# Optimization experiments

Measured on AMD Instinct MI355X. Metric: run time of the kernel, lower is better.

## Reference

```python
import jax, jax.numpy as jnp
import numpy as np

N = 100001          # 1000 DAGs * (99 tasks + 1 summary) + 1 global node
E = 3200000
IN_DIM = 8
H = 64
N_DAGS = 1000
TEMPERATURE = 1.0


def setup_inputs() -> dict:
    key = jax.random.key(0)
    ks = jax.random.split(key, 12)
    x = jax.random.normal(ks[0], (N, IN_DIM), dtype=jnp.float32)
    flags = jax.random.bernoulli(ks[1], 0.5, (N,)).astype(jnp.float32)
    x = x.at[:, -1].set(flags)  # last feature column is the schedule flag
    edge_index = jax.random.randint(ks[2], (2, E), 0, N, dtype=jnp.int32)
    dag_summary_index = jnp.arange(N_DAGS, dtype=jnp.int32) * 100 + 99

    def w(k, shape, fan_in):
        return jax.random.normal(k, shape, dtype=jnp.float32) / np.float32(np.sqrt(fan_in))

    return {
        'x': x,
        'edge_index': edge_index,
        'dag_summary_index': dag_summary_index,
        'W1': w(ks[3], (IN_DIM, H), IN_DIM), 'b1': jnp.zeros((H,), jnp.float32),
        'W2': w(ks[4], (H, H), H),           'b2': jnp.zeros((H,), jnp.float32),
        'M1': w(ks[5], (3 * H, H), 3 * H),   'mb1': jnp.zeros((H,), jnp.float32),
        'M2': w(ks[6], (H, H), H),           'mb2': jnp.zeros((H,), jnp.float32),
        'M3': w(ks[7], (H, 1), H),           'mb3': jnp.zeros((1,), jnp.float32),
    }


def _gcn_conv(x, src, dst, W, b):
    # PyG GCNConv: add self-loops, symmetric normalization, linear, scatter-add, bias
    n = x.shape[0]
    loop = jnp.arange(n, dtype=src.dtype)
    s = jnp.concatenate([src, loop])
    d = jnp.concatenate([dst, loop])
    deg = jax.ops.segment_sum(jnp.ones_like(s, dtype=x.dtype), d, num_segments=n)
    dinv = jnp.where(deg > 0, jax.lax.rsqrt(deg), 0.0)
    norm = dinv[s] * dinv[d]                      # [E+N]
    h = x @ W                                     # [N, H]
    msg = h[s] * norm[:, None]                    # gather + scale (memory-bound)
    return jax.ops.segment_sum(msg, d, num_segments=n) + b


def reference(x, edge_index, dag_summary_index, W1, b1, W2, b2, M1, mb1, M2, mb2, M3, mb3):
    src, dst = edge_index[0], edge_index[1]
    h = jax.nn.relu(_gcn_conv(x, src, dst, W1, b1))
    h = jax.nn.relu(_gcn_conv(h, src, dst, W2, b2))   # [N, H]

    n = x.shape[0]
    idx = jnp.arange(n - 1)
    # dag_idx for node i == number of summary indices <= i (matches loop increment)
    dag_of = jnp.searchsorted(dag_summary_index, idx, side='right')
    dag_of = jnp.clip(dag_of, 0, dag_summary_index.shape[0] - 1)
    dag_emb = h[dag_summary_index[dag_of]]            # [N-1, H]
    global_emb = jnp.broadcast_to(h[-1], (n - 1, h.shape[1]))
    combined = jnp.concatenate([h[:-1], dag_emb, global_emb], axis=1)  # [N-1, 3H]

    z = jax.nn.relu(combined @ M1 + mb1)
    z = jax.nn.relu(z @ M2 + mb2)
    scores = (z @ M3 + mb3)[:, 0]                     # [N-1]

    flags = x[:-1, -1]
    is_summary = jnp.zeros((n,), bool).at[dag_summary_index].set(True)[:-1]
    mask = (flags == 1.0) & (~is_summary)
    probs = jax.nn.softmax(jnp.where(mask, scores / TEMPERATURE, -jnp.inf))
    selected = jnp.argmax(probs)                      # is_sampling=False path
    return probs, selected
```

## Files before the change

kernel.cpp:

```cpp
#include <hip/hip_runtime.h>
#include <math.h>

#define CHUNK 8192


__global__ void __launch_bounds__(256) k_bcount(const int* __restrict__ dst, int e,
                                                int* __restrict__ bcount) {
    __shared__ int c[256];
    int t = threadIdx.x;
    c[t] = 0;
    __syncthreads();
    for (int i = blockIdx.x * 256 + t; i < e; i += gridDim.x * 256)
        atomicAdd(&c[dst[i] >> 9], 1);
    __syncthreads();
    if (c[t]) atomicAdd(&bcount[t], c[t]);
}

__global__ void k_bscan(const int* __restrict__ bcount, int nb, int e,
                        int* __restrict__ bbase, int* __restrict__ bcur) {
    __shared__ int s[256];
    int t = threadIdx.x;
    int v = (t < nb) ? bcount[t] : 0;
    s[t] = v;
    __syncthreads();
    for (int d = 1; d < 256; d <<= 1) {
        int a = (t >= d) ? s[t - d] : 0;
        __syncthreads();
        s[t] += a;
        __syncthreads();
    }
    if (t < nb) { bbase[t] = s[t] - v; bcur[t] = s[t] - v; }
    if (t == 0) bbase[nb] = e;
}

__global__ void __launch_bounds__(256) k_bscatter(const int* __restrict__ src,
                                                  const int* __restrict__ dst, int e,
                                                  int* __restrict__ bcur,
                                                  unsigned* __restrict__ eu) {
    __shared__ unsigned short rank[CHUNK];
    __shared__ int cnt[256];
    __shared__ int base[256];
    int t = threadIdx.x;
    int c0 = blockIdx.x * CHUNK;
    cnt[t] = 0;
    __syncthreads();
#pragma unroll
    for (int k = 0; k < CHUNK / 256; k++) {
        int i = c0 + k * 256 + t;
        if (i < e) {
            int b = dst[i] >> 9;
            rank[k * 256 + t] = (unsigned short)atomicAdd(&cnt[b], 1);
        }
    }
    __syncthreads();
    int cb = cnt[t];
    base[t] = cb ? atomicAdd(&bcur[t], cb) : 0;
    __syncthreads();
#pragma unroll
    for (int k = 0; k < CHUNK / 256; k++) {
        int i = c0 + k * 256 + t;
        if (i < e) {
            int d = dst[i];
            int b = d >> 9;
            eu[base[b] + rank[k * 256 + t]] =
                ((unsigned)src[i] << 9) | (unsigned)(d & 511);
        }
    }
}

__global__ void __launch_bounds__(256) k_bdeg(const unsigned* __restrict__ eu,
                                              const int* __restrict__ bbase,
                                              int* __restrict__ deg, int* __restrict__ off,
                                              float* __restrict__ dinv, int n) {
    __shared__ int h[512];
    int t = threadIdx.x, b = blockIdx.x;
    h[t] = 0; h[t + 256] = 0;
    __syncthreads();
    int s0 = bbase[b], s1 = bbase[b + 1];
    for (int i = s0 + t; i < s1; i += 256)
        atomicAdd(&h[eu[i] & 511u], 1);
    __syncthreads();
    int o0 = h[t], o1 = h[t + 256];
    for (int d = 1; d < 512; d <<= 1) {
        int a0 = (t >= d) ? h[t - d] : 0;
        int a1 = (t + 256 >= d) ? h[t + 256 - d] : 0;
        __syncthreads();
        h[t] += a0; h[t + 256] += a1;
        __syncthreads();
    }
    int nbase = b << 9;
    int n0 = nbase + t, n1 = nbase + t + 256;
    if (n0 < n) { deg[n0] = o0; off[n0] = s0 + h[t] - o0; dinv[n0] = rsqrtf((float)(o0 + 1)); }
    if (n1 < n) { deg[n1] = o1; off[n1] = s0 + h[t + 256] - o1; dinv[n1] = rsqrtf((float)(o1 + 1)); }
}

__global__ void __launch_bounds__(256) k_bcsr(const unsigned* __restrict__ eu,
                                              const int* __restrict__ bbase,
                                              const int* __restrict__ off,
                                              int* __restrict__ csr, int n) {
    __shared__ int curL[512];
    __shared__ int offL[512];
    int t = threadIdx.x, b = blockIdx.x;
    int nbase = b << 9;
    curL[t] = 0; curL[t + 256] = 0;
    int n0 = nbase + t, n1 = nbase + t + 256;
    offL[t] = (n0 < n) ? off[n0] : 0;
    offL[t + 256] = (n1 < n) ? off[n1] : 0;
    __syncthreads();
    int s0 = bbase[b], s1 = bbase[b + 1];
    for (int i = s0 + t; i < s1; i += 256) {
        unsigned p = eu[i];
        int local = (int)(p & 511u);
        int r = atomicAdd(&curL[local], 1);
        csr[offL[local] + r] = (int)(p >> 9);
    }
}


__global__ void k_xs(const float* __restrict__ x, const float* __restrict__ dinv,
                     float* __restrict__ xs, int n) {
    int t = blockIdx.x * blockDim.x + threadIdx.x;
    if (t >= n * 8) return;
    xs[t] = x[t] * dinv[t >> 3];
}


__global__ void __launch_bounds__(256) k_conv8(const float* __restrict__ xs,
                                               const int* __restrict__ csr,
                                               const int* __restrict__ off,
                                               const int* __restrict__ deg,
                                               float* __restrict__ agg1, int n) {
    int g = (blockIdx.x * 256 + threadIdx.x) >> 3;
    int lane = threadIdx.x & 7;
    if (g >= n) return;
    int base = off[g], cnt = deg[g];
    float acc = xs[g * 8 + lane];
    int e = 0;
    for (; e + 4 <= cnt; e += 4) {
        int s0 = csr[base + e];
        int s1 = csr[base + e + 1];
        int s2 = csr[base + e + 2];
        int s3 = csr[base + e + 3];
        acc += xs[s0 * 8 + lane];
        acc += xs[s1 * 8 + lane];
        acc += xs[s2 * 8 + lane];
        acc += xs[s3 * 8 + lane];
    }
    for (; e < cnt; e++) acc += xs[csr[base + e] * 8 + lane];
    agg1[g * 8 + lane] = acc;
}


__global__ void k_h1(const float* __restrict__ agg1, const float* __restrict__ W1,
                     const float* __restrict__ b1, const float* __restrict__ dinv,
                     float* __restrict__ H1s, int n) {
    int t = blockIdx.x * blockDim.x + threadIdx.x;
    int i = t >> 6, j = t & 63;
    if (i >= n) return;
    const float* ar = agg1 + (size_t)i * 8;
    float acc = 0.f;
#pragma unroll
    for (int k = 0; k < 8; k++) acc += ar[k] * W1[k * 64 + j];
    float dv = dinv[i];
    float h = fmaxf(dv * acc + b1[j], 0.f);
    H1s[(size_t)i * 64 + j] = h * dv;
}


__global__ void __launch_bounds__(256) k_conv64(const float* __restrict__ G,
                                                const int* __restrict__ csr,
                                                const int* __restrict__ off,
                                                const int* __restrict__ deg,
                                                float* __restrict__ agg2, int n) {
    int d = (blockIdx.x * 256 + threadIdx.x) >> 6;
    int j = threadIdx.x & 63;
    if (d >= n) return;
    int du = __builtin_amdgcn_readfirstlane(d);
    int base = off[du], cnt = deg[du];
    const float* Gj = G + j;
    float acc = Gj[(size_t)du * 64];
    int e = 0;
    for (; e + 8 <= cnt; e += 8) {
        int s[8];
#pragma unroll
        for (int u = 0; u < 8; u++) s[u] = csr[base + e + u];
        float v[8];
#pragma unroll
        for (int u = 0; u < 8; u++) v[u] = Gj[(size_t)s[u] * 64];
#pragma unroll
        for (int u = 0; u < 8; u++) acc += v[u];
    }
    for (; e < cnt; e++) acc += Gj[(size_t)csr[base + e] * 64];
    agg2[(size_t)d * 64 + j] = acc;
}


__global__ void __launch_bounds__(256) k_gw2b(const float* __restrict__ In,
                                              const float* __restrict__ W2,
                                              const float* __restrict__ b2,
                                              const float* __restrict__ dinv,
                                              float* __restrict__ Out, int n) {
    __shared__ float hs[128 * 65];
    __shared__ float ws[64 * 64];
    int tid = threadIdx.x;
    int base = blockIdx.x * 128;
#pragma unroll
    for (int m = 0; m < 4; m++) {
        int i = (m * 256 + tid) * 4;
        *(float4*)&ws[i] = *(const float4*)&W2[i];
    }
#pragma unroll
    for (int m = 0; m < 8; m++) {
        int idx = (m * 256 + tid) * 4;
        int node = idx >> 6, k = idx & 63;
        float4 v = *(const float4*)&In[(size_t)(base + node) * 64 + k];
        hs[node * 65 + k]     = v.x;
        hs[node * 65 + k + 1] = v.y;
        hs[node * 65 + k + 2] = v.z;
        hs[node * 65 + k + 3] = v.w;
    }
    __syncthreads();
    int jg = tid & 7, ng = tid >> 3;
    int j0 = jg * 8, n0 = ng * 4;
    float acc[4][8];
#pragma unroll
    for (int i = 0; i < 4; i++)
#pragma unroll
        for (int j = 0; j < 8; j++) acc[i][j] = 0.f;
#pragma unroll 4
    for (int k = 0; k < 64; k++) {
        float av[4];
#pragma unroll
        for (int i = 0; i < 4; i++) av[i] = hs[(n0 + i) * 65 + k];
        float bv[8];
        *(float4*)&bv[0] = *(float4*)&ws[k * 64 + j0];
        *(float4*)&bv[4] = *(float4*)&ws[k * 64 + j0 + 4];
#pragma unroll
        for (int i = 0; i < 4; i++)
#pragma unroll
            for (int j = 0; j < 8; j++) acc[i][j] += av[i] * bv[j];
    }
    float b2v[8];
    *(float4*)&b2v[0] = *(const float4*)&b2[j0];
    *(float4*)&b2v[4] = *(const float4*)&b2[j0 + 4];
#pragma unroll
    for (int i = 0; i < 4; i++) {
        int node = base + n0 + i;
        if (node < n) {
            float dv = dinv[node];
            float4 o0, o1;
            o0.x = fmaxf(acc[i][0] * dv + b2v[0], 0.f);
            o0.y = fmaxf(acc[i][1] * dv + b2v[1], 0.f);
            o0.z = fmaxf(acc[i][2] * dv + b2v[2], 0.f);
            o0.w = fmaxf(acc[i][3] * dv + b2v[3], 0.f);
            o1.x = fmaxf(acc[i][4] * dv + b2v[4], 0.f);
            o1.y = fmaxf(acc[i][5] * dv + b2v[5], 0.f);
            o1.z = fmaxf(acc[i][6] * dv + b2v[6], 0.f);
            o1.w = fmaxf(acc[i][7] * dv + b2v[7], 0.f);
            *(float4*)&Out[(size_t)node * 64 + j0]     = o0;
            *(float4*)&Out[(size_t)node * 64 + j0 + 4] = o1;
        }
    }
}


__global__ void k_dgt(const float* __restrict__ Hfin, const int* __restrict__ dsi,
                      const float* __restrict__ M1, const float* __restrict__ b1,
                      float* __restrict__ dgt, int n, int nd) {
    int w = (blockIdx.x * blockDim.x + threadIdx.x) >> 6;
    int lane = threadIdx.x & 63;
    if (w >= nd) return;
    float hd = Hfin[(size_t)dsi[w] * 64 + lane];
    float hg = Hfin[(size_t)(n - 1) * 64 + lane];
    float z = b1[lane];
#pragma unroll
    for (int k = 0; k < 64; k++) z += __shfl(hd, k) * M1[(64 + k) * 64 + lane];
#pragma unroll
    for (int k = 0; k < 64; k++) z += __shfl(hg, k) * M1[(128 + k) * 64 + lane];
    dgt[w * 64 + lane] = z;
}


__global__ void __launch_bounds__(256) k_mlp(const float* __restrict__ Hfin,
                                             const float* __restrict__ dgt,
                                             const float* __restrict__ x,
                                             const float* __restrict__ M1,
                                             const float* __restrict__ M2,
                                             const float* __restrict__ mb2,
                                             const float* __restrict__ M3,
                                             const float* __restrict__ mb3,
                                             float* __restrict__ scores, int n, int nd) {
    __shared__ float hs[128 * 65];
    __shared__ float ws[64 * 64];
    int tid = threadIdx.x;
    int base = blockIdx.x * 128;
#pragma unroll
    for (int m = 0; m < 4; m++) {
        int i = (m * 256 + tid) * 4;
        *(float4*)&ws[i] = *(const float4*)&M1[i];
    }
#pragma unroll
    for (int m = 0; m < 8; m++) {
        int idx = (m * 256 + tid) * 4;
        int node = idx >> 6, k = idx & 63;
        float4 v = *(const float4*)&Hfin[(size_t)(base + node) * 64 + k];
        hs[node * 65 + k]     = v.x;
        hs[node * 65 + k + 1] = v.y;
        hs[node * 65 + k + 2] = v.z;
        hs[node * 65 + k + 3] = v.w;
    }
    __syncthreads();
    int jg = tid & 7, ng = tid >> 3;
    int j0 = jg * 8, n0 = ng * 4;
    float acc[4][8];
#pragma unroll
    for (int i = 0; i < 4; i++)
#pragma unroll
        for (int j = 0; j < 8; j++) acc[i][j] = 0.f;
#pragma unroll 4
    for (int k = 0; k < 64; k++) {
        float av[4];
#pragma unroll
        for (int i = 0; i < 4; i++) av[i] = hs[(n0 + i) * 65 + k];
        float bv[8];
        *(float4*)&bv[0] = *(float4*)&ws[k * 64 + j0];
        *(float4*)&bv[4] = *(float4*)&ws[k * 64 + j0 + 4];
#pragma unroll
        for (int i = 0; i < 4; i++)
#pragma unroll
            for (int j = 0; j < 8; j++) acc[i][j] += av[i] * bv[j];
    }
    __syncthreads();
#pragma unroll
    for (int i = 0; i < 4; i++) {
        int node = base + n0 + i;
        int dago = (node + 1) / 100;
        if (dago >= nd) dago = nd - 1;
        float dv[8];
        *(float4*)&dv[0] = *(const float4*)&dgt[dago * 64 + j0];
        *(float4*)&dv[4] = *(const float4*)&dgt[dago * 64 + j0 + 4];
#pragma unroll
        for (int j = 0; j < 8; j++)
            hs[(n0 + i) * 65 + j0 + j] = fmaxf(acc[i][j] + dv[j], 0.f);
    }
#pragma unroll
    for (int m = 0; m < 4; m++) {
        int i = (m * 256 + tid) * 4;
        *(float4*)&ws[i] = *(const float4*)&M2[i];
    }
    __syncthreads();
    float acc2[4][8];
#pragma unroll
    for (int i = 0; i < 4; i++)
#pragma unroll
        for (int j = 0; j < 8; j++) acc2[i][j] = 0.f;
#pragma unroll 4
    for (int k = 0; k < 64; k++) {
        float av[4];
#pragma unroll
        for (int i = 0; i < 4; i++) av[i] = hs[(n0 + i) * 65 + k];
        float bv[8];
        *(float4*)&bv[0] = *(float4*)&ws[k * 64 + j0];
        *(float4*)&bv[4] = *(float4*)&ws[k * 64 + j0 + 4];
#pragma unroll
        for (int i = 0; i < 4; i++)
#pragma unroll
            for (int j = 0; j < 8; j++) acc2[i][j] += av[i] * bv[j];
    }
    float b2v[8], m3v[8];
    *(float4*)&b2v[0] = *(const float4*)&mb2[j0];
    *(float4*)&b2v[4] = *(const float4*)&mb2[j0 + 4];
    *(float4*)&m3v[0] = *(const float4*)&M3[j0];
    *(float4*)&m3v[4] = *(const float4*)&M3[j0 + 4];
    float b3 = mb3[0];
#pragma unroll
    for (int i = 0; i < 4; i++) {
        float p = 0.f;
#pragma unroll
        for (int j = 0; j < 8; j++) {
            float z2 = fmaxf(acc2[i][j] + b2v[j], 0.f);
            p += z2 * m3v[j];
        }
        p += __shfl_xor(p, 1);
        p += __shfl_xor(p, 2);
        p += __shfl_xor(p, 4);
        if (jg == 0) {
            int node = base + n0 + i;
            if (node < n - 1) {
                float flag = x[(size_t)node * 8 + 7];
                bool summary = ((node % 100) == 99);
                scores[node] = (flag == 1.0f && !summary) ? (p + b3) : -INFINITY;
            }
        }
    }
}


__global__ void k_red_ms(const float* __restrict__ scores, int n,
                         float* __restrict__ pm, float* __restrict__ ps,
                         int* __restrict__ pidx) {
    __shared__ float sm[256];
    __shared__ float ss[256];
    __shared__ int si[256];
    float m = -INFINITY, s = 0.f;
    int bi = 0x7fffffff;
    for (int i = blockIdx.x * 256 + threadIdx.x; i < n; i += gridDim.x * 256) {
        float v = scores[i];
        if (v > m) {
            s = s * expf(m - v) + 1.f;
            m = v;
            bi = i;
        } else if (v != -INFINITY) {
            s += expf(v - m);
        }
    }
    sm[threadIdx.x] = m; ss[threadIdx.x] = s; si[threadIdx.x] = bi;
    __syncthreads();
    for (int o = 128; o; o >>= 1) {
        if (threadIdx.x < o) {
            float m2 = sm[threadIdx.x + o], s2 = ss[threadIdx.x + o];
            int i2 = si[threadIdx.x + o];
            float m1 = sm[threadIdx.x], s1 = ss[threadIdx.x];
            int i1 = si[threadIdx.x];
            float M = fmaxf(m1, m2);
            float S = ((m1 == -INFINITY) ? 0.f : s1 * expf(m1 - M)) +
                      ((m2 == -INFINITY) ? 0.f : s2 * expf(m2 - M));
            int I;
            if (m2 > m1 || (m2 == m1 && i2 < i1)) I = i2; else I = i1;
            sm[threadIdx.x] = M; ss[threadIdx.x] = S; si[threadIdx.x] = I;
        }
        __syncthreads();
    }
    if (threadIdx.x == 0) { pm[blockIdx.x] = sm[0]; ps[blockIdx.x] = ss[0]; pidx[blockIdx.x] = si[0]; }
}

__global__ void k_red_comb(const float* __restrict__ pm, const float* __restrict__ ps,
                           const int* __restrict__ pidx, int nb,
                           float* __restrict__ finals, int* __restrict__ seli) {
    __shared__ float sm[256];
    __shared__ float ss[256];
    __shared__ int si[256];
    int t = threadIdx.x;
    sm[t] = (t < nb) ? pm[t] : -INFINITY;
    ss[t] = (t < nb) ? ps[t] : 0.f;
    si[t] = (t < nb) ? pidx[t] : 0x7fffffff;
    __syncthreads();
    for (int o = 128; o; o >>= 1) {
        if (t < o) {
            float m2 = sm[t + o], s2 = ss[t + o];
            int i2 = si[t + o];
            float m1 = sm[t], s1 = ss[t];
            int i1 = si[t];
            float M = fmaxf(m1, m2);
            float S = ((m1 == -INFINITY) ? 0.f : s1 * expf(m1 - M)) +
                      ((m2 == -INFINITY) ? 0.f : s2 * expf(m2 - M));
            int I;
            if (m2 > m1 || (m2 == m1 && i2 < i1)) I = i2; else I = i1;
            sm[t] = M; ss[t] = S; si[t] = I;
        }
        __syncthreads();
    }
    if (t == 0) { finals[0] = sm[0]; finals[1] = ss[0]; seli[0] = si[0]; }
}

__global__ void k_probs(const float* __restrict__ scores, const float* __restrict__ finals,
                        const int* __restrict__ seli, float* __restrict__ out, int n) {
    int i = blockIdx.x * 256 + threadIdx.x;
    float m = finals[0];
    float s = finals[1];
    if (i < n) out[i] = expf(scores[i] - m) / s;
    if (i == 0) out[n] = (float)seli[0];
}


extern "C" void kernel_launch(void* const* d_in, const int* in_sizes, int n_in,
                              void* d_out, int out_size, void* d_ws, size_t ws_size,
                              hipStream_t stream) {
    const float* x   = (const float*)d_in[0];
    const int*   ei  = (const int*)d_in[1];
    const int*   dsi = (const int*)d_in[2];
    const float* W1  = (const float*)d_in[3];
    const float* b1  = (const float*)d_in[4];
    const float* W2  = (const float*)d_in[5];
    const float* b2  = (const float*)d_in[6];
    const float* M1  = (const float*)d_in[7];
    const float* mb1 = (const float*)d_in[8];  (void)mb1;
    const float* M2  = (const float*)d_in[9];
    const float* mb2 = (const float*)d_in[10];
    const float* M3  = (const float*)d_in[11];
    const float* mb3 = (const float*)d_in[12];

    int N  = in_sizes[0] / 8;
    int E  = in_sizes[1] / 2;
    int ND = in_sizes[2];

    int N32 = (N + 63) & ~63;
    int NPAD = ((N + 127) / 128) * 128;
    int TILES = NPAD / 128;
    int nb = (N + 511) >> 9;

    char* p = (char*)d_ws;
    auto alloc = [&](size_t bytes) {
        char* r = p;
        p += (bytes + 255) & ~(size_t)255;
        return r;
    };
    int*   deg    = (int*)alloc((size_t)N32 * 4);
    int*   off    = (int*)alloc((size_t)N32 * 4);
    float* dinv   = (float*)alloc((size_t)N32 * 4);
    int*   csr    = (int*)alloc((size_t)E * 4);
    float* A      = (float*)alloc((size_t)NPAD * 64 * 4);
    float* B      = (float*)alloc((size_t)NPAD * 64 * 4);
    float* xs     = (float*)alloc((size_t)N32 * 8 * 4);
    float* agg1   = (float*)alloc((size_t)N32 * 8 * 4);
    float* dgt    = (float*)alloc((size_t)ND * 64 * 4);
    float* scores = (float*)alloc((size_t)N32 * 4);
    int*   bcount = (int*)alloc(256 * 4);
    int*   bbase  = (int*)alloc(257 * 4);
    int*   bcur   = (int*)alloc(256 * 4);
    float* pm     = (float*)alloc(256 * 4);
    float* ps     = (float*)alloc(256 * 4);
    int*   pidx   = (int*)alloc(256 * 4);
    float* finals = (float*)alloc(16 * 4);
    int*   seli   = (int*)alloc(16 * 4);
    if ((size_t)(p - (char*)d_ws) > ws_size) return;

    unsigned* eu = (unsigned*)A;

    const int* esrc = ei;
    const int* edst = ei + E;

    hipMemsetAsync(bcount, 0, 256 * 4, stream);
    k_bcount<<<512, 256, 0, stream>>>(edst, E, bcount);
    k_bscan<<<1, 256, 0, stream>>>(bcount, nb, E, bbase, bcur);
    k_bscatter<<<(E + CHUNK - 1) / CHUNK, 256, 0, stream>>>(esrc, edst, E, bcur, eu);
    k_bdeg<<<nb, 256, 0, stream>>>(eu, bbase, deg, off, dinv, N);
    k_bcsr<<<nb, 256, 0, stream>>>(eu, bbase, off, csr, N);

    k_xs<<<(N * 8 + 255) / 256, 256, 0, stream>>>(x, dinv, xs, N);
    k_conv8<<<(N * 8 + 255) / 256, 256, 0, stream>>>(xs, csr, off, deg, agg1, N);
    k_h1<<<(N * 64 + 255) / 256, 256, 0, stream>>>(agg1, W1, b1, dinv, A, N);

    k_conv64<<<(N + 3) / 4, 256, 0, stream>>>(A, csr, off, deg, B, N);
    k_gw2b<<<TILES, 256, 0, stream>>>(B, W2, b2, dinv, B, N);

    k_dgt<<<(ND * 64 + 255) / 256, 256, 0, stream>>>(B, dsi, M1, b1, dgt, N, ND);
    k_mlp<<<TILES, 256, 0, stream>>>(B, dgt, x, M1, M2, mb2, M3, mb3, scores, N, ND);

    int NS = N - 1;
    k_red_ms<<<256, 256, 0, stream>>>(scores, NS, pm, ps, pidx);
    k_red_comb<<<1, 256, 0, stream>>>(pm, ps, pidx, 256, finals, seli);
    k_probs<<<(NS + 256) / 256, 256, 0, stream>>>(scores, finals, seli, (float*)d_out, NS);
}
```

Before: 321.6 us.

## Split 64-wide GCN aggregation into two column-half passes with edge-split lanes

Replaces the single 64-column gather-sum kernel with two launches, each covering 32 feature columns. Within a wavefront the two 32-lane halves take alternating edges and are combined with a cross-lane shuffle. Each pass touches only half of each source row, which is meant to shrink the working set for better cache hit rates on the random gathers. The cost is reading the CSR index arrays twice and launching twice as many waves, each doing half the column work.

```diff
diff --git a/kernel.cpp b/kernel.cpp
--- a/kernel.cpp
+++ b/kernel.cpp
@@ -167,31 +167,36 @@
 }
 
 
-__global__ void __launch_bounds__(256) k_conv64(const float* __restrict__ G,
-                                                const int* __restrict__ csr,
-                                                const int* __restrict__ off,
-                                                const int* __restrict__ deg,
-                                                float* __restrict__ agg2, int n) {
-    int d = (blockIdx.x * 256 + threadIdx.x) >> 6;
-    int j = threadIdx.x & 63;
-    if (d >= n) return;
-    int du = __builtin_amdgcn_readfirstlane(d);
-    int base = off[du], cnt = deg[du];
-    const float* Gj = G + j;
-    float acc = Gj[(size_t)du * 64];
+__global__ void __launch_bounds__(256) k_conv64s(const float* __restrict__ G,
+                                                 const int* __restrict__ csr,
+                                                 const int* __restrict__ off,
+                                                 const int* __restrict__ deg,
+                                                 float* __restrict__ agg2, int n, int half) {
+    int w = (blockIdx.x * 256 + threadIdx.x) >> 6;
+    if (w >= n) return;
+    int lane = threadIdx.x & 63;
+    int es = lane >> 5;
+    int jj = (lane & 31) + half * 32;
+    int base = off[w], cnt = deg[w];
+    const float* Gj = G + jj;
+    float acc = (es == 0) ? Gj[(size_t)w * 64] : 0.f;
     int e = 0;
-    for (; e + 8 <= cnt; e += 8) {
+    for (; e + 16 <= cnt; e += 16) {
         int s[8];
 #pragma unroll
-        for (int u = 0; u < 8; u++) s[u] = csr[base + e + u];
+        for (int u = 0; u < 8; u++) s[u] = csr[base + e + 2 * u + es];
         float v[8];
 #pragma unroll
         for (int u = 0; u < 8; u++) v[u] = Gj[(size_t)s[u] * 64];
 #pragma unroll
         for (int u = 0; u < 8; u++) acc += v[u];
     }
-    for (; e < cnt; e++) acc += Gj[(size_t)csr[base + e] * 64];
-    agg2[(size_t)d * 64 + j] = acc;
+    for (; e + 2 <= cnt; e += 2)
+        acc += Gj[(size_t)csr[base + e + es] * 64];
+    if (e < cnt && es == 0)
+        acc += Gj[(size_t)csr[base + e] * 64];
+    acc += __shfl_xor(acc, 32);
+    if (es == 0) agg2[(size_t)w * 64 + jj] = acc;
 }
 
 
@@ -541,7 +546,8 @@
     k_conv8<<<(N * 8 + 255) / 256, 256, 0, stream>>>(xs, csr, off, deg, agg1, N);
     k_h1<<<(N * 64 + 255) / 256, 256, 0, stream>>>(agg1, W1, b1, dinv, A, N);
 
-    k_conv64<<<(N + 3) / 4, 256, 0, stream>>>(A, csr, off, deg, B, N);
+    k_conv64s<<<(N + 3) / 4, 256, 0, stream>>>(A, csr, off, deg, B, N, 0);
+    k_conv64s<<<(N + 3) / 4, 256, 0, stream>>>(A, csr, off, deg, B, N, 1);
     k_gw2b<<<TILES, 256, 0, stream>>>(B, W2, b2, dinv, B, N);
 
     k_dgt<<<(ND * 64 + 255) / 256, 256, 0, stream>>>(B, dsi, M1, b1, dgt, N, ND);
```

Result: slower. 357.8 us (+11.2%).

## Pre-sort bucket edges by source range and fuse degree, CSR and xs kernels

Applied to the files above, without the earlier changes.

Adds a per-bucket counting sort on the high bits of the source id, so that each CSR row's neighbour list comes out in roughly ascending source order. This should give the later gather kernels better locality. The degree/offset kernel, the CSR fill kernel and the xs scaling kernel are merged into one per-bucket kernel that keeps dinv in shared memory. The cost is an extra full pass that reads and writes the edge array through the B buffer, and atomic ordering inside a bucket still leaves rows only partially sorted.

```diff
diff --git a/kernel.cpp b/kernel.cpp
--- a/kernel.cpp
+++ b/kernel.cpp
@@ -68,13 +68,48 @@
     }
 }
 
-__global__ void __launch_bounds__(256) k_bdeg(const unsigned* __restrict__ eu,
-                                              const int* __restrict__ bbase,
-                                              int* __restrict__ deg, int* __restrict__ off,
-                                              float* __restrict__ dinv, int n) {
+__global__ void __launch_bounds__(256) k_bsort(const unsigned* __restrict__ eu,
+                                               const int* __restrict__ bbase,
+                                               unsigned* __restrict__ ebuf) {
+    __shared__ int hist[256];
+    __shared__ int cur[256];
+    int t = threadIdx.x, b = blockIdx.x;
+    hist[t] = 0;
+    __syncthreads();
+    int s0 = bbase[b], s1 = bbase[b + 1];
+    for (int i = s0 + t; i < s1; i += 256)
+        atomicAdd(&hist[eu[i] >> 18], 1);
+    __syncthreads();
+    int v = hist[t];
+    __syncthreads();
+    for (int d = 1; d < 256; d <<= 1) {
+        int a = (t >= d) ? hist[t - d] : 0;
+        __syncthreads();
+        hist[t] += a;
+        __syncthreads();
+    }
+    cur[t] = hist[t] - v;
+    __syncthreads();
+    for (int i = s0 + t; i < s1; i += 256) {
+        unsigned p = eu[i];
+        int r = atomicAdd(&cur[p >> 18], 1);
+        ebuf[s0 + r] = p;
+    }
+}
+
+__global__ void __launch_bounds__(256) k_bprep(const unsigned* __restrict__ eu,
+                                               const int* __restrict__ bbase,
+                                               const float* __restrict__ x,
+                                               int* __restrict__ deg, int* __restrict__ off,
+                                               float* __restrict__ dinv, float* __restrict__ xs,
+                                               int* __restrict__ csr, int n) {
     __shared__ int h[512];
+    __shared__ int offL[512];
+    __shared__ int curL[512];
+    __shared__ float sdv[512];
     int t = threadIdx.x, b = blockIdx.x;
     h[t] = 0; h[t + 256] = 0;
+    curL[t] = 0; curL[t + 256] = 0;
     __syncthreads();
     int s0 = bbase[b], s1 = bbase[b + 1];
     for (int i = s0 + t; i < s1; i += 256)
@@ -90,38 +125,27 @@
     }
     int nbase = b << 9;
     int n0 = nbase + t, n1 = nbase + t + 256;
-    if (n0 < n) { deg[n0] = o0; off[n0] = s0 + h[t] - o0; dinv[n0] = rsqrtf((float)(o0 + 1)); }
-    if (n1 < n) { deg[n1] = o1; off[n1] = s0 + h[t + 256] - o1; dinv[n1] = rsqrtf((float)(o1 + 1)); }
-}
-
-__global__ void __launch_bounds__(256) k_bcsr(const unsigned* __restrict__ eu,
-                                              const int* __restrict__ bbase,
-                                              const int* __restrict__ off,
-                                              int* __restrict__ csr, int n) {
-    __shared__ int curL[512];
-    __shared__ int offL[512];
-    int t = threadIdx.x, b = blockIdx.x;
-    int nbase = b << 9;
-    curL[t] = 0; curL[t + 256] = 0;
-    int n0 = nbase + t, n1 = nbase + t + 256;
-    offL[t] = (n0 < n) ? off[n0] : 0;
-    offL[t + 256] = (n1 < n) ? off[n1] : 0;
-    __syncthreads();
-    int s0 = bbase[b], s1 = bbase[b + 1];
+    int ofA = s0 + h[t] - o0, ofB = s0 + h[t + 256] - o1;
+    offL[t] = ofA; offL[t + 256] = ofB;
+    if (n0 < n) {
+        float dv = rsqrtf((float)(o0 + 1));
+        deg[n0] = o0; off[n0] = ofA; dinv[n0] = dv; sdv[t] = dv;
+    }
+    if (n1 < n) {
+        float dv = rsqrtf((float)(o1 + 1));
+        deg[n1] = o1; off[n1] = ofB; dinv[n1] = dv; sdv[t + 256] = dv;
+    }
+    __syncthreads();
+    int limit = (n - nbase) * 8;
+    if (limit > 4096) limit = 4096;
+    for (int idx = t; idx < limit; idx += 256)
+        xs[(size_t)nbase * 8 + idx] = x[(size_t)nbase * 8 + idx] * sdv[idx >> 3];
     for (int i = s0 + t; i < s1; i += 256) {
         unsigned p = eu[i];
         int local = (int)(p & 511u);
         int r = atomicAdd(&curL[local], 1);
         csr[offL[local] + r] = (int)(p >> 9);
     }
-}
-
-
-__global__ void k_xs(const float* __restrict__ x, const float* __restrict__ dinv,
-                     float* __restrict__ xs, int n) {
-    int t = blockIdx.x * blockDim.x + threadIdx.x;
-    if (t >= n * 8) return;
-    xs[t] = x[t] * dinv[t >> 3];
 }
 
 
@@ -525,7 +549,8 @@
     int*   seli   = (int*)alloc(16 * 4);
     if ((size_t)(p - (char*)d_ws) > ws_size) return;
 
-    unsigned* eu = (unsigned*)A;
+    unsigned* eu   = (unsigned*)A;
+    unsigned* ebuf = (unsigned*)B;
 
     const int* esrc = ei;
     const int* edst = ei + E;
@@ -534,10 +559,9 @@
     k_bcount<<<512, 256, 0, stream>>>(edst, E, bcount);
     k_bscan<<<1, 256, 0, stream>>>(bcount, nb, E, bbase, bcur);
     k_bscatter<<<(E + CHUNK - 1) / CHUNK, 256, 0, stream>>>(esrc, edst, E, bcur, eu);
-    k_bdeg<<<nb, 256, 0, stream>>>(eu, bbase, deg, off, dinv, N);
-    k_bcsr<<<nb, 256, 0, stream>>>(eu, bbase, off, csr, N);
-
-    k_xs<<<(N * 8 + 255) / 256, 256, 0, stream>>>(x, dinv, xs, N);
+    k_bsort<<<nb, 256, 0, stream>>>(eu, bbase, ebuf);
+    k_bprep<<<nb, 256, 0, stream>>>(ebuf, bbase, x, deg, off, dinv, xs, csr, N);
+
     k_conv8<<<(N * 8 + 255) / 256, 256, 0, stream>>>(xs, csr, off, deg, agg1, N);
     k_h1<<<(N * 64 + 255) / 256, 256, 0, stream>>>(agg1, W1, b1, dinv, A, N);
 
```

Result: slower. 358.3 us (+11.4%).
